# Kernel tuning notes

Measured on AMD Instinct MI355X. Metric: run time of the kernel, lower is better.

The kernel has to match this reference:

```python
import jax, jax.numpy as jnp
import numpy as np

V, E, H, B = 32000, 1024, 2048, 512


def setup_inputs() -> dict:
    key = jax.random.key(0)
    ks = jax.random.split(key, 9)
    s = 0.02
    emb_table = jax.random.normal(ks[0], (V, E), jnp.float32) * s
    emb_table = emb_table.at[0].set(0.0)  # padding_idx=0
    W_ih = jax.random.normal(ks[1], (3 * H, E), jnp.float32) * s  # gates [r,z,n]
    W_hh = jax.random.normal(ks[2], (3 * H, H), jnp.float32) * s
    b_ih = jax.random.normal(ks[3], (3 * H,), jnp.float32) * s
    b_hh = jax.random.normal(ks[4], (3 * H,), jnp.float32) * s
    fc_W = jax.random.normal(ks[5], (V, H), jnp.float32) * s
    fc_b = jax.random.normal(ks[6], (V,), jnp.float32) * s
    input_step = jax.random.randint(ks[7], (B,), 0, V, jnp.int64)
    hidden = jax.random.normal(ks[8], (1, B, H), jnp.float32)
    return {"input_step": input_step, "hidden": hidden, "emb_table": emb_table,
            "W_ih": W_ih, "W_hh": W_hh, "b_ih": b_ih, "b_hh": b_hh,
            "fc_W": fc_W, "fc_b": fc_b}


def reference(input_step, hidden, emb_table, W_ih, W_hh, b_ih, b_hh, fc_W, fc_b):
    # Embedding lookup (seq_len=1, so the unsqueeze/squeeze cancel)
    x = emb_table[input_step]                       # [B, E]
    h = hidden[0]                                   # [B, H]
    # Single GRU step, PyTorch gate order [r, z, n]
    gi = x @ W_ih.T + b_ih                          # [B, 3H]
    gh = h @ W_hh.T + b_hh                          # [B, 3H]
    gi_r, gi_z, gi_n = jnp.split(gi, 3, axis=-1)
    gh_r, gh_z, gh_n = jnp.split(gh, 3, axis=-1)
    r = jax.nn.sigmoid(gi_r + gh_r)
    z = jax.nn.sigmoid(gi_z + gh_z)
    n = jnp.tanh(gi_n + r * gh_n)
    h_new = (1.0 - z) * n + z * h                   # [B, H]
    logits = h_new @ fc_W.T + fc_b                  # [B, V]
    return logits, h_new[None]                      # hidden back as [1, B, H]
```

## Files before the change

kernel.cpp:

```cpp
#include <hip/hip_runtime.h>
#include <hip/hip_bf16.h>

typedef __attribute__((ext_vector_type(8))) short short8;
typedef __attribute__((ext_vector_type(4))) short short4v;
typedef __attribute__((ext_vector_type(4))) float f32x4;

__device__ __forceinline__ short f2bf(float f) {
  union { __hip_bfloat16 h; short s; } u;
  u.h = __float2bfloat16(f);
  return u.s;
}

__device__ __forceinline__ int swz(int row, int scol) {
  return row * 64 + (scol ^ ((row & 7) << 3));
}

template<int BN_>
__device__ __forceinline__ void gemm_body(
    const short* __restrict__ A,
    const float* __restrict__ W,
    const float* __restrict__ bias,
    float* __restrict__ C,
    int K, int N, int nb)
{
  constexpr int BF  = BN_ / 16;
  constexpr int TPR = 512 / BN_;
  constexpr int FPT = 64 / TPR;
  __shared__ short lds[2][BN_ * 64];

  const int t    = threadIdx.x;
  const int wave = t >> 6;
  const int lane = t & 63;
  const int l16  = lane & 15;
  const int lq   = lane >> 4;
  const int n0   = nb * BN_;

  const int sv = t / TPR;
  const int sk = (t % TPR) * FPT;
  const float* wp = W + (size_t)(n0 + sv) * K + sk;

  f32x4 acc[4][BF];
  #pragma unroll
  for (int i = 0; i < 4; ++i)
    #pragma unroll
    for (int j = 0; j < BF; ++j) {
      f32x4 z = {0.f, 0.f, 0.f, 0.f};
      acc[i][j] = z;
    }

  const short* aBase = A + (size_t)(wave * 64 + l16) * K + lq * 8;

  f32x4 wreg[FPT / 4];

  #pragma unroll
  for (int i = 0; i < FPT / 4; ++i) wreg[i] = *(const f32x4*)(wp + i * 4);
  #pragma unroll
  for (int j = 0; j < FPT / 8; ++j) {
    short8 wb;
    #pragma unroll
    for (int i = 0; i < 8; ++i) wb[i] = f2bf(wreg[j * 2 + (i >> 2)][i & 3]);
    *(short8*)&lds[0][swz(sv, sk + j * 8)] = wb;
  }
  __syncthreads();

  const int nt = K >> 6;
  for (int tI = 0; tI < nt; ++tI) {
    if (tI + 1 < nt) {
      #pragma unroll
      for (int i = 0; i < FPT / 4; ++i)
        wreg[i] = *(const f32x4*)(wp + (tI + 1) * 64 + i * 4);
    }

    const short* lbuf = lds[tI & 1];
    const int kb = tI << 6;
    #pragma unroll
    for (int ks = 0; ks < 2; ++ks) {
      short8 a[4], b[BF];
      #pragma unroll
      for (int mf = 0; mf < 4; ++mf)
        a[mf] = *(const short8*)(aBase + (size_t)mf * 16 * K + kb + ks * 32);
      #pragma unroll
      for (int nf = 0; nf < BF; ++nf)
        b[nf] = *(const short8*)&lbuf[swz(nf * 16 + l16, ks * 32 + lq * 8)];
      #pragma unroll
      for (int mf = 0; mf < 4; ++mf)
        #pragma unroll
        for (int nf = 0; nf < BF; ++nf)
          acc[mf][nf] = __builtin_amdgcn_mfma_f32_16x16x32_bf16(a[mf], b[nf], acc[mf][nf], 0, 0, 0);
    }

    if (tI + 1 < nt) {
      short* lw = (short*)lds[(tI + 1) & 1];
      #pragma unroll
      for (int j = 0; j < FPT / 8; ++j) {
        short8 wb;
        #pragma unroll
        for (int i = 0; i < 8; ++i) wb[i] = f2bf(wreg[j * 2 + (i >> 2)][i & 3]);
        *(short8*)&lw[swz(sv, sk + j * 8)] = wb;
      }
    }
    __syncthreads();
  }

  #pragma unroll
  for (int nf = 0; nf < BF; ++nf) {
    const int col = n0 + nf * 16 + l16;
    const float bv = bias[col];
    #pragma unroll
    for (int mf = 0; mf < 4; ++mf) {
      const int row = wave * 64 + mf * 16 + lq * 4;
      #pragma unroll
      for (int r = 0; r < 4; ++r)
        C[(size_t)(row + r) * N + col] = acc[mf][nf][r] + bv;
    }
  }
}

__global__ __launch_bounds__(512, 2) void gru_gemms_kernel(
    const short* __restrict__ xbf, const short* __restrict__ hbf,
    const float* __restrict__ W_ih, const float* __restrict__ W_hh,
    const float* __restrict__ b_ih, const float* __restrict__ b_hh,
    float* __restrict__ gi, float* __restrict__ gh)
{
  const bool second = blockIdx.x >= 96;
  gemm_body<64>(second ? hbf : xbf,
                second ? W_hh : W_ih,
                second ? b_hh : b_ih,
                second ? gh : gi,
                second ? 2048 : 1024,
                6144,
                second ? (int)blockIdx.x - 96 : (int)blockIdx.x);
}

__global__ __launch_bounds__(512, 2) void logits_kernel(
    const short* __restrict__ hnbf, const float* __restrict__ fc_W,
    const float* __restrict__ fc_b, float* __restrict__ out)
{
  gemm_body<128>(hnbf, fc_W, fc_b, out, 2048, 32000, (int)blockIdx.x);
}

__global__ void prep_kernel(const int* __restrict__ idx,
                            const float* __restrict__ hid,
                            const float* __restrict__ emb,
                            short* __restrict__ xbf, short* __restrict__ hbf)
{
  int i = blockIdx.x * blockDim.x + threadIdx.x;
  const int NX = 512 * 1024 / 4;
  const int NH = 512 * 2048 / 4;
  if (i < NX) {
    int b = i >> 8;
    int c = (i & 255) << 2;
    int row = idx[b];
    f32x4 v = *(const f32x4*)(emb + (size_t)row * 1024 + c);
    short4v o;
    #pragma unroll
    for (int j = 0; j < 4; ++j) o[j] = f2bf(v[j]);
    *(short4v*)(xbf + (size_t)b * 1024 + c) = o;
  } else if (i < NX + NH) {
    int j2 = i - NX;
    f32x4 v = *(const f32x4*)(hid + (size_t)j2 * 4);
    short4v o;
    #pragma unroll
    for (int j = 0; j < 4; ++j) o[j] = f2bf(v[j]);
    *(short4v*)(hbf + (size_t)j2 * 4) = o;
  }
}

__global__ void gates_kernel(const float* __restrict__ gi,
                             const float* __restrict__ gh,
                             const float* __restrict__ hid,
                             float* __restrict__ hnew,
                             short* __restrict__ hnbf)
{
  int i = blockIdx.x * blockDim.x + threadIdx.x;
  int b = i >> 9;
  int c = (i & 511) << 2;
  size_t gbase = (size_t)b * 6144 + c;
  f32x4 gir = *(const f32x4*)(gi + gbase);
  f32x4 giz = *(const f32x4*)(gi + gbase + 2048);
  f32x4 gin = *(const f32x4*)(gi + gbase + 4096);
  f32x4 ghr = *(const f32x4*)(gh + gbase);
  f32x4 ghz = *(const f32x4*)(gh + gbase + 2048);
  f32x4 ghn = *(const f32x4*)(gh + gbase + 4096);
  f32x4 hv  = *(const f32x4*)(hid + (size_t)b * 2048 + c);
  f32x4 hn;
  short4v hb;
  #pragma unroll
  for (int j = 0; j < 4; ++j) {
    float r = 1.f / (1.f + __expf(-(gir[j] + ghr[j])));
    float z = 1.f / (1.f + __expf(-(giz[j] + ghz[j])));
    float n = tanhf(gin[j] + r * ghn[j]);
    float o = (1.f - z) * n + z * hv[j];
    hn[j] = o;
    hb[j] = f2bf(o);
  }
  *(f32x4*)(hnew + (size_t)b * 2048 + c) = hn;
  *(short4v*)(hnbf + (size_t)b * 2048 + c) = hb;
}

extern "C" void kernel_launch(void* const* d_in, const int* in_sizes, int n_in,
                              void* d_out, int out_size, void* d_ws, size_t ws_size,
                              hipStream_t stream)
{
  const int*   idx   = (const int*)d_in[0];
  const float* hid   = (const float*)d_in[1];
  const float* emb   = (const float*)d_in[2];
  const float* W_ih  = (const float*)d_in[3];
  const float* W_hh  = (const float*)d_in[4];
  const float* b_ih  = (const float*)d_in[5];
  const float* b_hh  = (const float*)d_in[6];
  const float* fc_W  = (const float*)d_in[7];
  const float* fc_b  = (const float*)d_in[8];
  float* out = (float*)d_out;

  char* ws = (char*)d_ws;
  short* xbf  = (short*)(ws);
  short* hbf  = (short*)(ws + 1048576);
  short* hnbf = (short*)(ws + 3145728);
  float* gi   = (float*)(ws + 5242880);
  float* gh   = (float*)(ws + 17825792);

  prep_kernel<<<1536, 256, 0, stream>>>(idx, hid, emb, xbf, hbf);
  gru_gemms_kernel<<<192, 512, 0, stream>>>(xbf, hbf, W_ih, W_hh, b_ih, b_hh, gi, gh);
  gates_kernel<<<1024, 256, 0, stream>>>(gi, gh, hid, out + (size_t)512 * 32000, hnbf);
  logits_kernel<<<250, 512, 0, stream>>>(hnbf, fc_W, fc_b, out);
}
```

Baseline: 229.5 us.

## Prefetch weight tiles two steps ahead with ping-pong register buffers

Measured after the change: 259.0 us. 1.13x slower.

```diff
diff --git a/kernel.cpp b/kernel.cpp
--- a/kernel.cpp
+++ b/kernel.cpp
@@ -26,6 +26,7 @@
   constexpr int BF  = BN_ / 16;
   constexpr int TPR = 512 / BN_;
   constexpr int FPT = 64 / TPR;
+  constexpr int NV  = FPT / 4;
   __shared__ short lds[2][BN_ * 64];
 
   const int t    = threadIdx.x;
@@ -50,57 +51,65 @@
 
   const short* aBase = A + (size_t)(wave * 64 + l16) * K + lq * 8;
 
-  f32x4 wreg[FPT / 4];
-
-  #pragma unroll
-  for (int i = 0; i < FPT / 4; ++i) wreg[i] = *(const f32x4*)(wp + i * 4);
-  #pragma unroll
-  for (int j = 0; j < FPT / 8; ++j) {
-    short8 wb;
-    #pragma unroll
-    for (int i = 0; i < 8; ++i) wb[i] = f2bf(wreg[j * 2 + (i >> 2)][i & 3]);
-    *(short8*)&lds[0][swz(sv, sk + j * 8)] = wb;
-  }
-  __syncthreads();
+  f32x4 wa[NV], wb[NV];
+
+  auto issue = [&](f32x4 (&S)[NV], int tile) {
+    #pragma unroll
+    for (int i = 0; i < NV; ++i)
+      S[i] = *(const f32x4*)(wp + tile * 64 + i * 4);
+  };
+  auto commit = [&](f32x4 (&S)[NV], int buf) {
+    short* lw = (short*)lds[buf];
+    #pragma unroll
+    for (int j = 0; j < FPT / 8; ++j) {
+      short8 v;
+      #pragma unroll
+      for (int i = 0; i < 8; ++i) v[i] = f2bf(S[j * 2 + (i >> 2)][i & 3]);
+      *(short8*)&lw[swz(sv, sk + j * 8)] = v;
+    }
+  };
 
   const int nt = K >> 6;
-  for (int tI = 0; tI < nt; ++tI) {
-    if (tI + 1 < nt) {
-      #pragma unroll
-      for (int i = 0; i < FPT / 4; ++i)
-        wreg[i] = *(const f32x4*)(wp + (tI + 1) * 64 + i * 4);
-    }
-
-    const short* lbuf = lds[tI & 1];
-    const int kb = tI << 6;
-    #pragma unroll
-    for (int ks = 0; ks < 2; ++ks) {
-      short8 a[4], b[BF];
-      #pragma unroll
-      for (int mf = 0; mf < 4; ++mf)
-        a[mf] = *(const short8*)(aBase + (size_t)mf * 16 * K + kb + ks * 32);
-      #pragma unroll
-      for (int nf = 0; nf < BF; ++nf)
-        b[nf] = *(const short8*)&lbuf[swz(nf * 16 + l16, ks * 32 + lq * 8)];
-      #pragma unroll
-      for (int mf = 0; mf < 4; ++mf)
-        #pragma unroll
-        for (int nf = 0; nf < BF; ++nf)
-          acc[mf][nf] = __builtin_amdgcn_mfma_f32_16x16x32_bf16(a[mf], b[nf], acc[mf][nf], 0, 0, 0);
-    }
-
-    if (tI + 1 < nt) {
-      short* lw = (short*)lds[(tI + 1) & 1];
-      #pragma unroll
-      for (int j = 0; j < FPT / 8; ++j) {
-        short8 wb;
-        #pragma unroll
-        for (int i = 0; i < 8; ++i) wb[i] = f2bf(wreg[j * 2 + (i >> 2)][i & 3]);
-        *(short8*)&lw[swz(sv, sk + j * 8)] = wb;
-      }
-    }
-    __syncthreads();
-  }
+
+  issue(wa, 0);
+  issue(wb, 1);
+  commit(wa, 0);
+  asm volatile("s_waitcnt lgkmcnt(0)" ::: "memory");
+  __builtin_amdgcn_s_barrier();
+
+#define GSTEP(T, WI, WC)                                                      \
+  {                                                                           \
+    const int kb_ = (T) << 6;                                                 \
+    short8 a_[2][4];                                                          \
+    _Pragma("unroll")                                                         \
+    for (int ks = 0; ks < 2; ++ks)                                            \
+      _Pragma("unroll")                                                       \
+      for (int mf = 0; mf < 4; ++mf)                                          \
+        a_[ks][mf] = *(const short8*)(aBase + (size_t)mf * 16 * K + kb_ + ks * 32); \
+    if ((T) + 2 < nt) issue(WI, (T) + 2);                                     \
+    const short* lbuf_ = lds[(T) & 1];                                        \
+    _Pragma("unroll")                                                         \
+    for (int ks = 0; ks < 2; ++ks) {                                          \
+      short8 b_[BF];                                                          \
+      _Pragma("unroll")                                                       \
+      for (int nf = 0; nf < BF; ++nf)                                         \
+        b_[nf] = *(const short8*)&lbuf_[swz(nf * 16 + l16, ks * 32 + lq * 8)]; \
+      _Pragma("unroll")                                                       \
+      for (int mf = 0; mf < 4; ++mf)                                          \
+        _Pragma("unroll")                                                     \
+        for (int nf = 0; nf < BF; ++nf)                                       \
+          acc[mf][nf] = __builtin_amdgcn_mfma_f32_16x16x32_bf16(a_[ks][mf], b_[nf], acc[mf][nf], 0, 0, 0); \
+    }                                                                         \
+    if ((T) + 1 < nt) commit(WC, ((T) + 1) & 1);                              \
+    asm volatile("s_waitcnt lgkmcnt(0)" ::: "memory");                        \
+    __builtin_amdgcn_s_barrier();                                             \
+  }
+
+  for (int tI = 0; tI < nt; tI += 2) {
+    GSTEP(tI,     wa, wb)
+    GSTEP(tI + 1, wb, wa)
+  }
+#undef GSTEP
 
   #pragma unroll
   for (int nf = 0; nf < BF; ++nf) {
```
